# Performance work log

Hardware: AMD Instinct MI355X
Metric: run time of the kernel (lower is better)

## Reference

```python
import jax, jax.numpy as jnp
import numpy as np

N = 100000
E = 1000000
IN_C, HID, OUT_C = 64, 64, 40


def setup_inputs() -> dict:
    key = jax.random.key(0)
    ks = jax.random.split(key, 12)
    x = jax.random.normal(ks[0], (N, IN_C), dtype=jnp.float32)
    edge_index = jax.random.randint(ks[1], (2, E), 0, N, dtype=jnp.int64)

    def glorot(k, fan_in, fan_out):
        s = (6.0 / (fan_in + fan_out)) ** 0.5
        return jax.random.uniform(k, (fan_in, fan_out), jnp.float32, -s, s)

    return {
        "x": x,
        "edge_index": edge_index,
        "W1": glorot(ks[2], IN_C, HID), "b1": jnp.zeros((HID,), jnp.float32),
        "W2": glorot(ks[3], HID, HID), "b2": jnp.zeros((HID,), jnp.float32),
        "Wm1": glorot(ks[4], HID, HID), "bm1": jnp.zeros((HID,), jnp.float32),
        "Wm2": glorot(ks[5], HID, OUT_C), "bm2": jnp.zeros((OUT_C,), jnp.float32),
    }


def _gcn_conv(h_in, W, b, src, dst, deg_inv_sqrt):
    # PyG GCNConv: x' = D^{-1/2} (A + I) D^{-1/2} (x W) + b, self-loops added.
    h = h_in @ W                                        # [N, F]
    norm = deg_inv_sqrt[src] * deg_inv_sqrt[dst]        # [E]
    msg = h[src] * norm[:, None]                        # gather + scale
    agg = jax.ops.segment_sum(msg, dst, num_segments=N)  # scatter-add
    # self-loop contribution: deg_i^{-1/2} * deg_i^{-1/2} * h_i
    agg = agg + h * (deg_inv_sqrt * deg_inv_sqrt)[:, None]
    return agg + b


def reference(x, edge_index, W1, b1, W2, b2, Wm1, bm1, Wm2, bm2):
    src, dst = edge_index[0], edge_index[1]
    deg = jax.ops.segment_sum(jnp.ones((E,), jnp.float32), dst, num_segments=N) + 1.0
    deg_inv_sqrt = jax.lax.rsqrt(deg)

    h = _gcn_conv(x, W1, b1, src, dst, deg_inv_sqrt)
    h = jax.nn.relu(h)
    h = _gcn_conv(h, W2, b2, src, dst, deg_inv_sqrt)  # no relu after last conv

    h = jax.nn.relu(h @ Wm1 + bm1)
    out = h @ Wm2 + bm2
    return out
```

## Files before the change

kernel.cpp:

```cpp
#include <hip/hip_runtime.h>
#include <hip/hip_bf16.h>
#include <hip/hip_fp16.h>


namespace {

constexpr int N_NODES = 100000;
constexpr int N_EDGES = 1000000;
constexpr int NBUCK = (N_NODES + 511) / 512;
constexpr int CAP = 8192;
constexpr int EPB_A = 2048;

__global__ __launch_bounds__(256) void zero_detect_kernel(int* bucketCnt, int* flag,
                                                          const unsigned int* __restrict__ w) {
  int t = threadIdx.x;
  if (t < NBUCK) bucketCnt[t] = 0;
  if (t == 0) *flag = 0;
  __syncthreads();
  unsigned any = 0;
  for (int s = 0; s < 8; s++) {
    long long pos = ((long long)(t * 8 + s) * 104729LL) % N_EDGES;
    any |= w[2 * pos + 1];
  }
  if (any) atomicOr(flag, 1);
}

__global__ __launch_bounds__(256) void bucket_kernel(const void* __restrict__ ei,
                                                     const int* __restrict__ flag,
                                                     int* __restrict__ bucketCnt,
                                                     unsigned* __restrict__ tmp) {
  __shared__ int hist[NBUCK];
  __shared__ int basePB[NBUCK];
  __shared__ int cur[NBUCK];
  int t = threadIdx.x;
  if (t < NBUCK) { hist[t] = 0; cur[t] = 0; }
  __syncthreads();

  int e0 = blockIdx.x * EPB_A;
  int is32 = *flag;
  unsigned wreg[8];
  int breg[8];
#pragma unroll
  for (int k = 0; k < 8; k++) {
    int e = e0 + k * 256 + t;
    breg[k] = -1;
    if (e < N_EDGES) {
      int s, d;
      if (is32) {
        const int* p = (const int*)ei;
        s = p[e]; d = p[N_EDGES + e];
      } else {
        const long long* p = (const long long*)ei;
        s = (int)p[e]; d = (int)p[N_EDGES + e];
      }
      wreg[k] = ((unsigned)s << 9) | (unsigned)(d & 511);
      breg[k] = d >> 9;
      atomicAdd(&hist[breg[k]], 1);
    }
  }
  __syncthreads();
  if (t < NBUCK) basePB[t] = hist[t] ? atomicAdd(&bucketCnt[t], hist[t]) : 0;
  __syncthreads();
#pragma unroll
  for (int k = 0; k < 8; k++) {
    if (breg[k] >= 0) {
      int r = atomicAdd(&cur[breg[k]], 1);
      tmp[(size_t)breg[k] * CAP + basePB[breg[k]] + r] = wreg[k];
    }
  }
}

__global__ __launch_bounds__(512) void csr_kernel(const unsigned* __restrict__ tmp,
                                                  const int* __restrict__ bucketCnt,
                                                  int* __restrict__ col,
                                                  int* __restrict__ row_start,
                                                  int* __restrict__ row_end,
                                                  float* __restrict__ dinv) {
  __shared__ int sc[512];
  __shared__ int hist[512];
  __shared__ unsigned stage[CAP];
  int b = blockIdx.x, t = threadIdx.x;
  int myCnt = bucketCnt[b];
  int base = b * CAP;

  hist[t] = 0;
  __syncthreads();
  for (int i = t; i < myCnt; i += 512) {
    unsigned w = tmp[(size_t)base + i];
    stage[i] = w;
    atomicAdd(&hist[w & 511u], 1);
  }
  __syncthreads();

  int deg = hist[t];
  int pdeg = (deg + 7) & ~7;
  sc[t] = pdeg;
  __syncthreads();
#pragma unroll
  for (int off = 1; off < 512; off <<= 1) {
    int u = (t >= off) ? sc[t - off] : 0;
    __syncthreads();
    sc[t] += u;
    __syncthreads();
  }
  int pexcl = sc[t] - pdeg;
  int d = b * 512 + t;
  if (d < N_NODES) {
    row_start[d] = base + pexcl;
    row_end[d] = base + pexcl + pdeg;
    dinv[d] = rsqrtf((float)deg + 1.0f);
  }
  __syncthreads();
  hist[t] = pexcl;
  __syncthreads();
  for (int i = t; i < myCnt; i += 512) {
    unsigned w = stage[i];
    int pos = atomicAdd(&hist[w & 511u], 1);
    col[base + pos] = (int)(w >> 9);
  }
  for (int j = deg; j < pdeg; j++) col[base + pexcl + j] = N_NODES;
}

__device__ inline uint4 pack_half8(const float* v) {
  __half2 h0 = __floats2half2_rn(v[0], v[1]);
  __half2 h1 = __floats2half2_rn(v[2], v[3]);
  __half2 h2 = __floats2half2_rn(v[4], v[5]);
  __half2 h3 = __floats2half2_rn(v[6], v[7]);
  uint4 u;
  u.x = *(unsigned*)&h0; u.y = *(unsigned*)&h1;
  u.z = *(unsigned*)&h2; u.w = *(unsigned*)&h3;
  return u;
}

__global__ __launch_bounds__(256) void gemm_g_kernel(const float* __restrict__ A,
                                                     const float* __restrict__ W,
                                                     const float* __restrict__ dinv,
                                                     __half* __restrict__ g,
                                                     int reluIn) {
  __shared__ float Ws[64 * 64];
  int t = threadIdx.x;
  if (blockIdx.x == 0 && t < 32) ((float*)(g + (size_t)N_NODES * 64))[t] = 0.f;
  for (int i = t; i < 64 * 64 / 4; i += 256) ((float4*)Ws)[i] = ((const float4*)W)[i];
  __syncthreads();

  int rg = t >> 3, cg = t & 7;
  int r0 = blockIdx.x * 128 + rg * 4;
  int c0 = cg * 8;

  float acc[4][8];
#pragma unroll
  for (int i = 0; i < 4; i++)
#pragma unroll
    for (int j = 0; j < 8; j++) acc[i][j] = 0.f;

  const float4* A4 = (const float4*)A;
  for (int kk = 0; kk < 16; kk++) {
    float4 a[4];
#pragma unroll
    for (int i = 0; i < 4; i++) {
      int r = r0 + i;
      float4 v = (r < N_NODES) ? A4[(size_t)r * 16 + kk] : make_float4(0.f, 0.f, 0.f, 0.f);
      if (reluIn) {
        v.x = fmaxf(v.x, 0.f); v.y = fmaxf(v.y, 0.f);
        v.z = fmaxf(v.z, 0.f); v.w = fmaxf(v.w, 0.f);
      }
      a[i] = v;
    }
#pragma unroll
    for (int q = 0; q < 4; q++) {
      int k = kk * 4 + q;
      float w[8];
#pragma unroll
      for (int j = 0; j < 2; j++) *(float4*)&w[4 * j] = *(const float4*)&Ws[k * 64 + c0 + 4 * j];
#pragma unroll
      for (int i = 0; i < 4; i++) {
        float av = q == 0 ? a[i].x : q == 1 ? a[i].y : q == 2 ? a[i].z : a[i].w;
#pragma unroll
        for (int j = 0; j < 8; j++) acc[i][j] = fmaf(av, w[j], acc[i][j]);
      }
    }
  }
#pragma unroll
  for (int i = 0; i < 4; i++) {
    int r = r0 + i;
    if (r < N_NODES) {
      float s = dinv[r];
#pragma unroll
      for (int j = 0; j < 8; j++) acc[i][j] *= s;
      *(uint4*)(g + (size_t)r * 64 + c0) = pack_half8(acc[i]);
    }
  }
}

__global__ __launch_bounds__(256) void aggregate_kernel(const __half* __restrict__ g,
                                                        const int* __restrict__ col,
                                                        const int* __restrict__ row_start,
                                                        const int* __restrict__ row_end,
                                                        const float* __restrict__ dinv,
                                                        const float* __restrict__ bias,
                                                        float* __restrict__ out) {
  int wave = threadIdx.x >> 6;
  int lane = threadIdx.x & 63;
  int half = lane >> 5;
  int sub = lane & 31;
  int d = blockIdx.x * 8 + wave * 2 + half;

  const __half2* g2 = (const __half2*)g;
  int e0 = row_start[d];
  int len = row_end[d] - e0;

  float2 a0 = __half22float2(g2[(size_t)d * 32 + sub]);
  float2 a1 = {0.f, 0.f}, a2 = {0.f, 0.f}, a3 = {0.f, 0.f};
  float2 a4 = {0.f, 0.f}, a5 = {0.f, 0.f}, a6 = {0.f, 0.f}, a7 = {0.f, 0.f};

  for (int i = 0; i < len; i += 8) {
    int4 ca = *(const int4*)(col + e0 + i);
    int4 cb = *(const int4*)(col + e0 + i + 4);
    float2 h0 = __half22float2(g2[(size_t)ca.x * 32 + sub]);
    float2 h1 = __half22float2(g2[(size_t)ca.y * 32 + sub]);
    float2 h2 = __half22float2(g2[(size_t)ca.z * 32 + sub]);
    float2 h3 = __half22float2(g2[(size_t)ca.w * 32 + sub]);
    float2 h4 = __half22float2(g2[(size_t)cb.x * 32 + sub]);
    float2 h5 = __half22float2(g2[(size_t)cb.y * 32 + sub]);
    float2 h6 = __half22float2(g2[(size_t)cb.z * 32 + sub]);
    float2 h7 = __half22float2(g2[(size_t)cb.w * 32 + sub]);
    a0.x += h0.x; a0.y += h0.y; a1.x += h1.x; a1.y += h1.y;
    a2.x += h2.x; a2.y += h2.y; a3.x += h3.x; a3.y += h3.y;
    a4.x += h4.x; a4.y += h4.y; a5.x += h5.x; a5.y += h5.y;
    a6.x += h6.x; a6.y += h6.y; a7.x += h7.x; a7.y += h7.y;
  }
  float rx = ((a0.x + a1.x) + (a2.x + a3.x)) + ((a4.x + a5.x) + (a6.x + a7.x));
  float ry = ((a0.y + a1.y) + (a2.y + a3.y)) + ((a4.y + a5.y) + (a6.y + a7.y));
  float dv = dinv[d];
  float2 bv = ((const float2*)bias)[sub];
  float2 o;
  o.x = fmaf(rx, dv, bv.x);
  o.y = fmaf(ry, dv, bv.y);
  ((float2*)out)[(size_t)d * 32 + sub] = o;
}

template <int F>
__global__ __launch_bounds__(256) void gemm_kernel(const float* __restrict__ A, const float* __restrict__ W,
                                                   const float* __restrict__ bias, float* __restrict__ C,
                                                   int n, int reluIn, int reluOut) {
  constexpr int CPT = F / 8;
  __shared__ float Ws[64 * F];
  int t = threadIdx.x;
  for (int i = t; i < 64 * F / 4; i += 256) ((float4*)Ws)[i] = ((const float4*)W)[i];
  __syncthreads();

  int rg = t >> 3, cg = t & 7;
  int r0 = blockIdx.x * 128 + rg * 4;
  int c0 = cg * CPT;

  float acc[4][CPT];
#pragma unroll
  for (int i = 0; i < 4; i++)
#pragma unroll
    for (int j = 0; j < CPT; j++) acc[i][j] = 0.f;

  const float4* A4 = (const float4*)A;
  for (int kk = 0; kk < 16; kk++) {
    float4 a[4];
#pragma unroll
    for (int i = 0; i < 4; i++) {
      int r = r0 + i;
      float4 v = (r < n) ? A4[(size_t)r * 16 + kk] : make_float4(0.f, 0.f, 0.f, 0.f);
      if (reluIn) {
        v.x = fmaxf(v.x, 0.f); v.y = fmaxf(v.y, 0.f);
        v.z = fmaxf(v.z, 0.f); v.w = fmaxf(v.w, 0.f);
      }
      a[i] = v;
    }
#pragma unroll
    for (int q = 0; q < 4; q++) {
      int k = kk * 4 + q;
      float w[CPT];
      if constexpr (CPT % 4 == 0) {
#pragma unroll
        for (int j = 0; j < CPT / 4; j++)
          *(float4*)&w[4 * j] = *(const float4*)&Ws[k * F + c0 + 4 * j];
      } else {
#pragma unroll
        for (int j = 0; j < CPT; j++) w[j] = Ws[k * F + c0 + j];
      }
#pragma unroll
      for (int i = 0; i < 4; i++) {
        float av = q == 0 ? a[i].x : q == 1 ? a[i].y : q == 2 ? a[i].z : a[i].w;
#pragma unroll
        for (int j = 0; j < CPT; j++) acc[i][j] = fmaf(av, w[j], acc[i][j]);
      }
    }
  }

  float bv[CPT];
#pragma unroll
  for (int j = 0; j < CPT; j++) bv[j] = bias ? bias[c0 + j] : 0.f;
#pragma unroll
  for (int i = 0; i < 4; i++) {
    int r = r0 + i;
    if (r < n) {
      float* crow = C + (size_t)r * F + c0;
#pragma unroll
      for (int j = 0; j < CPT; j++) {
        float v = acc[i][j] + bv[j];
        if (reluOut) v = fmaxf(v, 0.f);
        crow[j] = v;
      }
    }
  }
}

}

extern "C" void kernel_launch(void* const* d_in, const int* in_sizes, int n_in,
                              void* d_out, int out_size, void* d_ws, size_t ws_size,
                              hipStream_t stream) {
  const float* x   = (const float*)d_in[0];
  const void*  ei  = d_in[1];
  const float* W1  = (const float*)d_in[2];
  const float* b1  = (const float*)d_in[3];
  const float* W2  = (const float*)d_in[4];
  const float* b2  = (const float*)d_in[5];
  const float* Wm1 = (const float*)d_in[6];
  const float* bm1 = (const float*)d_in[7];
  const float* Wm2 = (const float*)d_in[8];
  const float* bm2 = (const float*)d_in[9];
  float* out = (float*)d_out;

  char* ws = (char*)d_ws;
  size_t off = 0;
  auto alloc = [&](size_t bytes) -> void* {
    void* p = ws + off;
    off = (off + bytes + 511) & ~(size_t)511;
    return p;
  };
  int*      flag      = (int*)     alloc(4);
  int*      bucketCnt = (int*)     alloc((size_t)NBUCK * 4);
  unsigned* tmp       = (unsigned*)alloc((size_t)NBUCK * CAP * 4);
  int*      colA      = (int*)     alloc((size_t)NBUCK * CAP * 4);
  int*      rowS      = (int*)     alloc((size_t)N_NODES * 4);
  int*      rowE      = (int*)     alloc((size_t)N_NODES * 4);
  float*    dinv      = (float*)   alloc((size_t)N_NODES * 4);
  __half*   g1        = (__half*)  alloc((size_t)(N_NODES + 1) * 64 * 2);
  float*    hA        = (float*)   alloc((size_t)N_NODES * 64 * 4);
  float*    hB        = (float*)   alloc((size_t)N_NODES * 64 * 4);
  (void)ws_size; (void)in_sizes; (void)n_in; (void)out_size;

  dim3 b256(256);
  int gGemm = (N_NODES + 127) / 128;
  int gAgg  = N_NODES / 8;
  int gBkt  = (N_EDGES + EPB_A - 1) / EPB_A;

  zero_detect_kernel<<<1, b256, 0, stream>>>(bucketCnt, flag, (const unsigned int*)ei);
  bucket_kernel<<<gBkt, b256, 0, stream>>>(ei, flag, bucketCnt, tmp);
  csr_kernel<<<NBUCK, dim3(512), 0, stream>>>(tmp, bucketCnt, colA, rowS, rowE, dinv);

  gemm_g_kernel<<<gGemm, b256, 0, stream>>>(x, W1, dinv, g1, 0);
  aggregate_kernel<<<gAgg, b256, 0, stream>>>(g1, colA, rowS, rowE, dinv, b1, hB);

  gemm_g_kernel<<<gGemm, b256, 0, stream>>>(hB, W2, dinv, g1, 1);
  aggregate_kernel<<<gAgg, b256, 0, stream>>>(g1, colA, rowS, rowE, dinv, b2, hB);

  gemm_kernel<64><<<gGemm, b256, 0, stream>>>(hB, Wm1, bm1, hA, N_NODES, 0, 1);
  gemm_kernel<40><<<gGemm, b256, 0, stream>>>(hA, Wm2, bm2, out, N_NODES, 0, 0);
}
```

Baseline: 255.8 us.

## Store intermediate activations in fp16 and widen aggregation to 4 halves per lane

Intermediate feature buffers (aggregation outputs and the MLP hidden layer) are now stored as fp16 instead of fp32, and the GEMMs read fp16 inputs through a templated loader. The aggregation kernel now has each lane handle 4 halves via 8-byte loads, so a wave covers 4 nodes instead of 2. Bias is folded into the accumulator init, and the MLP GEMM reuses the fp16-output kernel. This roughly halves memory traffic for the intermediates, at the cost of extra fp16 rounding error in activations.

```diff
diff --git a/kernel.cpp b/kernel.cpp
--- a/kernel.cpp
+++ b/kernel.cpp
@@ -132,14 +132,33 @@
   return u;
 }
 
-__global__ __launch_bounds__(256) void gemm_g_kernel(const float* __restrict__ A,
+__device__ inline float4 h4tof4(uint2 u) {
+  float2 f0 = __half22float2(*(__half2*)&u.x);
+  float2 f1 = __half22float2(*(__half2*)&u.y);
+  return make_float4(f0.x, f0.y, f1.x, f1.y);
+}
+
+template <typename AT>
+__device__ inline float4 load4(const AT* A, size_t idx);
+template <>
+__device__ inline float4 load4<float>(const float* A, size_t idx) {
+  return ((const float4*)A)[idx];
+}
+template <>
+__device__ inline float4 load4<__half>(const __half* A, size_t idx) {
+  return h4tof4(((const uint2*)A)[idx]);
+}
+
+template <typename AT>
+__global__ __launch_bounds__(256) void gemm_h_kernel(const AT* __restrict__ A,
                                                      const float* __restrict__ W,
-                                                     const float* __restrict__ dinv,
+                                                     const float* __restrict__ bias,
+                                                     const float* __restrict__ rowScale,
                                                      __half* __restrict__ g,
-                                                     int reluIn) {
+                                                     int reluIn, int reluOut, int padZero) {
   __shared__ float Ws[64 * 64];
   int t = threadIdx.x;
-  if (blockIdx.x == 0 && t < 32) ((float*)(g + (size_t)N_NODES * 64))[t] = 0.f;
+  if (padZero && blockIdx.x == 0 && t < 32) ((float*)(g + (size_t)N_NODES * 64))[t] = 0.f;
   for (int i = t; i < 64 * 64 / 4; i += 256) ((float4*)Ws)[i] = ((const float4*)W)[i];
   __syncthreads();
 
@@ -151,15 +170,14 @@
 #pragma unroll
   for (int i = 0; i < 4; i++)
 #pragma unroll
-    for (int j = 0; j < 8; j++) acc[i][j] = 0.f;
-
-  const float4* A4 = (const float4*)A;
+    for (int j = 0; j < 8; j++) acc[i][j] = bias ? bias[c0 + j] : 0.f;
+
   for (int kk = 0; kk < 16; kk++) {
     float4 a[4];
 #pragma unroll
     for (int i = 0; i < 4; i++) {
       int r = r0 + i;
-      float4 v = (r < N_NODES) ? A4[(size_t)r * 16 + kk] : make_float4(0.f, 0.f, 0.f, 0.f);
+      float4 v = (r < N_NODES) ? load4(A, (size_t)r * 16 + kk) : make_float4(0.f, 0.f, 0.f, 0.f);
       if (reluIn) {
         v.x = fmaxf(v.x, 0.f); v.y = fmaxf(v.y, 0.f);
         v.z = fmaxf(v.z, 0.f); v.w = fmaxf(v.w, 0.f);
@@ -184,9 +202,13 @@
   for (int i = 0; i < 4; i++) {
     int r = r0 + i;
     if (r < N_NODES) {
-      float s = dinv[r];
-#pragma unroll
-      for (int j = 0; j < 8; j++) acc[i][j] *= s;
+      float s = rowScale ? rowScale[r] : 1.0f;
+#pragma unroll
+      for (int j = 0; j < 8; j++) {
+        float v = acc[i][j];
+        if (reluOut) v = fmaxf(v, 0.f);
+        acc[i][j] = v * s;
+      }
       *(uint4*)(g + (size_t)r * 64 + c0) = pack_half8(acc[i]);
     }
   }
@@ -198,55 +220,64 @@
                                                         const int* __restrict__ row_end,
                                                         const float* __restrict__ dinv,
                                                         const float* __restrict__ bias,
-                                                        float* __restrict__ out) {
+                                                        __half* __restrict__ out) {
   int wave = threadIdx.x >> 6;
   int lane = threadIdx.x & 63;
-  int half = lane >> 5;
-  int sub = lane & 31;
-  int d = blockIdx.x * 8 + wave * 2 + half;
-
-  const __half2* g2 = (const __half2*)g;
+  int quarter = lane >> 4;
+  int sub = lane & 15;
+  int d = blockIdx.x * 16 + wave * 4 + quarter;
+
+  const uint2* g4 = (const uint2*)g;
   int e0 = row_start[d];
   int len = row_end[d] - e0;
 
-  float2 a0 = __half22float2(g2[(size_t)d * 32 + sub]);
-  float2 a1 = {0.f, 0.f}, a2 = {0.f, 0.f}, a3 = {0.f, 0.f};
-  float2 a4 = {0.f, 0.f}, a5 = {0.f, 0.f}, a6 = {0.f, 0.f}, a7 = {0.f, 0.f};
+  float4 a0 = h4tof4(g4[(size_t)d * 16 + sub]);
+  float4 a1 = {0,0,0,0}, a2 = {0,0,0,0}, a3 = {0,0,0,0};
+  float4 a4 = {0,0,0,0}, a5 = {0,0,0,0}, a6 = {0,0,0,0}, a7 = {0,0,0,0};
 
   for (int i = 0; i < len; i += 8) {
     int4 ca = *(const int4*)(col + e0 + i);
     int4 cb = *(const int4*)(col + e0 + i + 4);
-    float2 h0 = __half22float2(g2[(size_t)ca.x * 32 + sub]);
-    float2 h1 = __half22float2(g2[(size_t)ca.y * 32 + sub]);
-    float2 h2 = __half22float2(g2[(size_t)ca.z * 32 + sub]);
-    float2 h3 = __half22float2(g2[(size_t)ca.w * 32 + sub]);
-    float2 h4 = __half22float2(g2[(size_t)cb.x * 32 + sub]);
-    float2 h5 = __half22float2(g2[(size_t)cb.y * 32 + sub]);
-    float2 h6 = __half22float2(g2[(size_t)cb.z * 32 + sub]);
-    float2 h7 = __half22float2(g2[(size_t)cb.w * 32 + sub]);
-    a0.x += h0.x; a0.y += h0.y; a1.x += h1.x; a1.y += h1.y;
-    a2.x += h2.x; a2.y += h2.y; a3.x += h3.x; a3.y += h3.y;
-    a4.x += h4.x; a4.y += h4.y; a5.x += h5.x; a5.y += h5.y;
-    a6.x += h6.x; a6.y += h6.y; a7.x += h7.x; a7.y += h7.y;
-  }
-  float rx = ((a0.x + a1.x) + (a2.x + a3.x)) + ((a4.x + a5.x) + (a6.x + a7.x));
-  float ry = ((a0.y + a1.y) + (a2.y + a3.y)) + ((a4.y + a5.y) + (a6.y + a7.y));
+    float4 h0 = h4tof4(g4[(size_t)ca.x * 16 + sub]);
+    float4 h1 = h4tof4(g4[(size_t)ca.y * 16 + sub]);
+    float4 h2 = h4tof4(g4[(size_t)ca.z * 16 + sub]);
+    float4 h3 = h4tof4(g4[(size_t)ca.w * 16 + sub]);
+    float4 h4v = h4tof4(g4[(size_t)cb.x * 16 + sub]);
+    float4 h5 = h4tof4(g4[(size_t)cb.y * 16 + sub]);
+    float4 h6 = h4tof4(g4[(size_t)cb.z * 16 + sub]);
+    float4 h7 = h4tof4(g4[(size_t)cb.w * 16 + sub]);
+    a0.x += h0.x; a0.y += h0.y; a0.z += h0.z; a0.w += h0.w;
+    a1.x += h1.x; a1.y += h1.y; a1.z += h1.z; a1.w += h1.w;
+    a2.x += h2.x; a2.y += h2.y; a2.z += h2.z; a2.w += h2.w;
+    a3.x += h3.x; a3.y += h3.y; a3.z += h3.z; a3.w += h3.w;
+    a4.x += h4v.x; a4.y += h4v.y; a4.z += h4v.z; a4.w += h4v.w;
+    a5.x += h5.x; a5.y += h5.y; a5.z += h5.z; a5.w += h5.w;
+    a6.x += h6.x; a6.y += h6.y; a6.z += h6.z; a6.w += h6.w;
+    a7.x += h7.x; a7.y += h7.y; a7.z += h7.z; a7.w += h7.w;
+  }
   float dv = dinv[d];
-  float2 bv = ((const float2*)bias)[sub];
-  float2 o;
-  o.x = fmaf(rx, dv, bv.x);
-  o.y = fmaf(ry, dv, bv.y);
-  ((float2*)out)[(size_t)d * 32 + sub] = o;
-}
-
-template <int F>
-__global__ __launch_bounds__(256) void gemm_kernel(const float* __restrict__ A, const float* __restrict__ W,
-                                                   const float* __restrict__ bias, float* __restrict__ C,
-                                                   int n, int reluIn, int reluOut) {
-  constexpr int CPT = F / 8;
-  __shared__ float Ws[64 * F];
+  float4 bv = ((const float4*)bias)[sub];
+  float o[4];
+  o[0] = fmaf(((a0.x + a1.x) + (a2.x + a3.x)) + ((a4.x + a5.x) + (a6.x + a7.x)), dv, bv.x);
+  o[1] = fmaf(((a0.y + a1.y) + (a2.y + a3.y)) + ((a4.y + a5.y) + (a6.y + a7.y)), dv, bv.y);
+  o[2] = fmaf(((a0.z + a1.z) + (a2.z + a3.z)) + ((a4.z + a5.z) + (a6.z + a7.z)), dv, bv.z);
+  o[3] = fmaf(((a0.w + a1.w) + (a2.w + a3.w)) + ((a4.w + a5.w) + (a6.w + a7.w)), dv, bv.w);
+  __half2 p0 = __floats2half2_rn(o[0], o[1]);
+  __half2 p1 = __floats2half2_rn(o[2], o[3]);
+  uint2 u;
+  u.x = *(unsigned*)&p0; u.y = *(unsigned*)&p1;
+  ((uint2*)out)[(size_t)d * 16 + sub] = u;
+}
+
+template <typename AT>
+__global__ __launch_bounds__(256) void gemm40_kernel(const AT* __restrict__ A,
+                                                     const float* __restrict__ W,
+                                                     const float* __restrict__ bias,
+                                                     float* __restrict__ C) {
+  constexpr int CPT = 5;
+  __shared__ float Ws[64 * 40];
   int t = threadIdx.x;
-  for (int i = t; i < 64 * F / 4; i += 256) ((float4*)Ws)[i] = ((const float4*)W)[i];
+  for (int i = t; i < 64 * 40 / 4; i += 256) ((float4*)Ws)[i] = ((const float4*)W)[i];
   __syncthreads();
 
   int rg = t >> 3, cg = t & 7;
@@ -257,33 +288,21 @@
 #pragma unroll
   for (int i = 0; i < 4; i++)
 #pragma unroll
-    for (int j = 0; j < CPT; j++) acc[i][j] = 0.f;
-
-  const float4* A4 = (const float4*)A;
+    for (int j = 0; j < CPT; j++) acc[i][j] = bias[c0 + j];
+
   for (int kk = 0; kk < 16; kk++) {
     float4 a[4];
 #pragma unroll
     for (int i = 0; i < 4; i++) {
       int r = r0 + i;
-      float4 v = (r < n) ? A4[(size_t)r * 16 + kk] : make_float4(0.f, 0.f, 0.f, 0.f);
-      if (reluIn) {
-        v.x = fmaxf(v.x, 0.f); v.y = fmaxf(v.y, 0.f);
-        v.z = fmaxf(v.z, 0.f); v.w = fmaxf(v.w, 0.f);
-      }
-      a[i] = v;
+      a[i] = (r < N_NODES) ? load4(A, (size_t)r * 16 + kk) : make_float4(0.f, 0.f, 0.f, 0.f);
     }
 #pragma unroll
     for (int q = 0; q < 4; q++) {
       int k = kk * 4 + q;
       float w[CPT];
-      if constexpr (CPT % 4 == 0) {
-#pragma unroll
-        for (int j = 0; j < CPT / 4; j++)
-          *(float4*)&w[4 * j] = *(const float4*)&Ws[k * F + c0 + 4 * j];
-      } else {
-#pragma unroll
-        for (int j = 0; j < CPT; j++) w[j] = Ws[k * F + c0 + j];
-      }
+#pragma unroll
+      for (int j = 0; j < CPT; j++) w[j] = Ws[k * 40 + c0 + j];
 #pragma unroll
       for (int i = 0; i < 4; i++) {
         float av = q == 0 ? a[i].x : q == 1 ? a[i].y : q == 2 ? a[i].z : a[i].w;
@@ -292,21 +311,13 @@
       }
     }
   }
-
-  float bv[CPT];
-#pragma unroll
-  for (int j = 0; j < CPT; j++) bv[j] = bias ? bias[c0 + j] : 0.f;
 #pragma unroll
   for (int i = 0; i < 4; i++) {
     int r = r0 + i;
-    if (r < n) {
-      float* crow = C + (size_t)r * F + c0;
-#pragma unroll
-      for (int j = 0; j < CPT; j++) {
-        float v = acc[i][j] + bv[j];
-        if (reluOut) v = fmaxf(v, 0.f);
-        crow[j] = v;
-      }
+    if (r < N_NODES) {
+      float* crow = C + (size_t)r * 40 + c0;
+#pragma unroll
+      for (int j = 0; j < CPT; j++) crow[j] = acc[i][j];
     }
   }
 }
@@ -343,25 +354,25 @@
   int*      rowE      = (int*)     alloc((size_t)N_NODES * 4);
   float*    dinv      = (float*)   alloc((size_t)N_NODES * 4);
   __half*   g1        = (__half*)  alloc((size_t)(N_NODES + 1) * 64 * 2);
-  float*    hA        = (float*)   alloc((size_t)N_NODES * 64 * 4);
-  float*    hB        = (float*)   alloc((size_t)N_NODES * 64 * 4);
+  __half*   hB        = (__half*)  alloc((size_t)N_NODES * 64 * 2);
+  __half*   hA        = (__half*)  alloc((size_t)N_NODES * 64 * 2);
   (void)ws_size; (void)in_sizes; (void)n_in; (void)out_size;
 
   dim3 b256(256);
   int gGemm = (N_NODES + 127) / 128;
-  int gAgg  = N_NODES / 8;
+  int gAgg  = N_NODES / 16;
   int gBkt  = (N_EDGES + EPB_A - 1) / EPB_A;
 
   zero_detect_kernel<<<1, b256, 0, stream>>>(bucketCnt, flag, (const unsigned int*)ei);
   bucket_kernel<<<gBkt, b256, 0, stream>>>(ei, flag, bucketCnt, tmp);
   csr_kernel<<<NBUCK, dim3(512), 0, stream>>>(tmp, bucketCnt, colA, rowS, rowE, dinv);
 
-  gemm_g_kernel<<<gGemm, b256, 0, stream>>>(x, W1, dinv, g1, 0);
+  gemm_h_kernel<float><<<gGemm, b256, 0, stream>>>(x, W1, nullptr, dinv, g1, 0, 0, 1);
   aggregate_kernel<<<gAgg, b256, 0, stream>>>(g1, colA, rowS, rowE, dinv, b1, hB);
 
-  gemm_g_kernel<<<gGemm, b256, 0, stream>>>(hB, W2, dinv, g1, 1);
+  gemm_h_kernel<__half><<<gGemm, b256, 0, stream>>>(hB, W2, nullptr, dinv, g1, 1, 0, 1);
   aggregate_kernel<<<gAgg, b256, 0, stream>>>(g1, colA, rowS, rowE, dinv, b2, hB);
 
-  gemm_kernel<64><<<gGemm, b256, 0, stream>>>(hB, Wm1, bm1, hA, N_NODES, 0, 1);
-  gemm_kernel<40><<<gGemm, b256, 0, stream>>>(hA, Wm2, bm2, out, N_NODES, 0, 0);
-}
+  gemm_h_kernel<__half><<<gGemm, b256, 0, stream>>>(hB, Wm1, bm1, nullptr, hA, 0, 1, 0);
+  gemm40_kernel<__half><<<gGemm, b256, 0, stream>>>(hA, Wm2, bm2, out);
+}
```

Result: slower. 271.4 us (+6.1%).

## Detect index width per block and pad CSR rows to four edges

Applied to the files above, without the earlier changes.

Drops the separate single-block detect kernel. Each bucket block now checks the high words of its own edges to decide between int32 and int64 indices, and bucketCnt is zeroed with a memset. Row padding in the CSR shrinks from multiples of 8 to multiples of 4, and the aggregate loop now handles 4 edges per iteration with 4 accumulators. This means fewer padded dummy gathers, at the cost of less memory-level parallelism per iteration. The per-block width check could disagree between blocks if some blocks happen to see only zero high words.

```diff
diff --git a/kernel.cpp b/kernel.cpp
--- a/kernel.cpp
+++ b/kernel.cpp
@@ -11,33 +11,30 @@
 constexpr int CAP = 8192;
 constexpr int EPB_A = 2048;
 
-__global__ __launch_bounds__(256) void zero_detect_kernel(int* bucketCnt, int* flag,
-                                                          const unsigned int* __restrict__ w) {
-  int t = threadIdx.x;
-  if (t < NBUCK) bucketCnt[t] = 0;
-  if (t == 0) *flag = 0;
-  __syncthreads();
-  unsigned any = 0;
-  for (int s = 0; s < 8; s++) {
-    long long pos = ((long long)(t * 8 + s) * 104729LL) % N_EDGES;
-    any |= w[2 * pos + 1];
-  }
-  if (any) atomicOr(flag, 1);
-}
-
 __global__ __launch_bounds__(256) void bucket_kernel(const void* __restrict__ ei,
-                                                     const int* __restrict__ flag,
                                                      int* __restrict__ bucketCnt,
                                                      unsigned* __restrict__ tmp) {
   __shared__ int hist[NBUCK];
   __shared__ int basePB[NBUCK];
   __shared__ int cur[NBUCK];
+  __shared__ int sflag;
   int t = threadIdx.x;
   if (t < NBUCK) { hist[t] = 0; cur[t] = 0; }
+  if (t == 0) sflag = 0;
   __syncthreads();
 
   int e0 = blockIdx.x * EPB_A;
-  int is32 = *flag;
+  const unsigned* w = (const unsigned*)ei;
+  unsigned any = 0;
+#pragma unroll
+  for (int s = 0; s < 2; s++) {
+    int e = e0 + s * 256 + t;
+    if (e < N_EDGES) any |= w[2 * e + 1];
+  }
+  if (any) sflag = 1;
+  __syncthreads();
+  int is32 = sflag;
+
   unsigned wreg[8];
   int breg[8];
 #pragma unroll
@@ -93,7 +90,7 @@
   __syncthreads();
 
   int deg = hist[t];
-  int pdeg = (deg + 7) & ~7;
+  int pdeg = (deg + 3) & ~3;
   sc[t] = pdeg;
   __syncthreads();
 #pragma unroll
@@ -211,26 +208,18 @@
 
   float2 a0 = __half22float2(g2[(size_t)d * 32 + sub]);
   float2 a1 = {0.f, 0.f}, a2 = {0.f, 0.f}, a3 = {0.f, 0.f};
-  float2 a4 = {0.f, 0.f}, a5 = {0.f, 0.f}, a6 = {0.f, 0.f}, a7 = {0.f, 0.f};
-
-  for (int i = 0; i < len; i += 8) {
+
+  for (int i = 0; i < len; i += 4) {
     int4 ca = *(const int4*)(col + e0 + i);
-    int4 cb = *(const int4*)(col + e0 + i + 4);
     float2 h0 = __half22float2(g2[(size_t)ca.x * 32 + sub]);
     float2 h1 = __half22float2(g2[(size_t)ca.y * 32 + sub]);
     float2 h2 = __half22float2(g2[(size_t)ca.z * 32 + sub]);
     float2 h3 = __half22float2(g2[(size_t)ca.w * 32 + sub]);
-    float2 h4 = __half22float2(g2[(size_t)cb.x * 32 + sub]);
-    float2 h5 = __half22float2(g2[(size_t)cb.y * 32 + sub]);
-    float2 h6 = __half22float2(g2[(size_t)cb.z * 32 + sub]);
-    float2 h7 = __half22float2(g2[(size_t)cb.w * 32 + sub]);
     a0.x += h0.x; a0.y += h0.y; a1.x += h1.x; a1.y += h1.y;
     a2.x += h2.x; a2.y += h2.y; a3.x += h3.x; a3.y += h3.y;
-    a4.x += h4.x; a4.y += h4.y; a5.x += h5.x; a5.y += h5.y;
-    a6.x += h6.x; a6.y += h6.y; a7.x += h7.x; a7.y += h7.y;
-  }
-  float rx = ((a0.x + a1.x) + (a2.x + a3.x)) + ((a4.x + a5.x) + (a6.x + a7.x));
-  float ry = ((a0.y + a1.y) + (a2.y + a3.y)) + ((a4.y + a5.y) + (a6.y + a7.y));
+  }
+  float rx = (a0.x + a1.x) + (a2.x + a3.x);
+  float ry = (a0.y + a1.y) + (a2.y + a3.y);
   float dv = dinv[d];
   float2 bv = ((const float2*)bias)[sub];
   float2 o;
@@ -335,7 +324,6 @@
     off = (off + bytes + 511) & ~(size_t)511;
     return p;
   };
-  int*      flag      = (int*)     alloc(4);
   int*      bucketCnt = (int*)     alloc((size_t)NBUCK * 4);
   unsigned* tmp       = (unsigned*)alloc((size_t)NBUCK * CAP * 4);
   int*      colA      = (int*)     alloc((size_t)NBUCK * CAP * 4);
@@ -352,8 +340,8 @@
   int gAgg  = N_NODES / 8;
   int gBkt  = (N_EDGES + EPB_A - 1) / EPB_A;
 
-  zero_detect_kernel<<<1, b256, 0, stream>>>(bucketCnt, flag, (const unsigned int*)ei);
-  bucket_kernel<<<gBkt, b256, 0, stream>>>(ei, flag, bucketCnt, tmp);
+  hipMemsetAsync(bucketCnt, 0, (size_t)NBUCK * 4, stream);
+  bucket_kernel<<<gBkt, b256, 0, stream>>>(ei, bucketCnt, tmp);
   csr_kernel<<<NBUCK, dim3(512), 0, stream>>>(tmp, bucketCnt, colA, rowS, rowE, dinv);
 
   gemm_g_kernel<<<gGemm, b256, 0, stream>>>(x, W1, dinv, g1, 0);
```

Result: slower. 263.5 us (+3.0%).
